# Kernel tuning notes

Hardware: AMD Instinct MI355X
Metric: run time of the kernel (lower is better)

Reference implementation:

```python
import jax, jax.numpy as jnp
import numpy as np

# Config (matches init_kwargs): num_ori=0 -> plain ConvNext path, single scale, knn-16 graph.
N, B, G, K = 16384, 8, 2048, 16   # N nodes = B graphs x G nodes, k-NN with self loops
C, BD, WF, L = 128, 128, 4, 4     # hidden, basis_dim, widening_factor, num layers
POLY_IN = 3                        # PolynomialFeatures(degree=2) on [E,1] dist -> [d, d^2, d^3]


def knn_edges(pos):
    # Graphs are contiguous blocks of G nodes (batch = node // G).
    pg = pos.reshape(B, G, 3)
    d2 = jnp.sum((pg[:, :, None, :] - pg[:, None, :, :]) ** 2, axis=-1)  # [B,G,G]
    _, idx = jax.lax.top_k(-d2, K)                                       # [B,G,K] incl. self (loop=True)
    offset = (jnp.arange(B) * G)[:, None, None]
    src = (idx + offset).reshape(-1)            # neighbor (source) node per edge, [E]
    dst = jnp.repeat(jnp.arange(B * G), K)      # center (target) node per edge, [E]
    return src, dst


def layer_norm(h, g, b):
    mu = jnp.mean(h, axis=-1, keepdims=True)
    var = jnp.var(h, axis=-1, keepdims=True)
    return (h - mu) / jnp.sqrt(var + 1e-5) * g + b


def setup_inputs() -> dict:
    key = jax.random.key(0)
    ks = jax.random.split(key, 20)
    s = 0.05
    inp = {
        'x': jax.random.normal(ks[0], (N, 65), jnp.float32),
        'pos': jax.random.normal(ks[1], (N, 3), jnp.float32),
        'batch': jnp.repeat(jnp.arange(B, dtype=jnp.int32), G),
        # x_embedder (no bias)
        'W_embed': jax.random.normal(ks[2], (65, C), jnp.float32) * s,
        # spatial basis MLP: poly(3) -> Linear -> GELU -> Linear -> GELU
        'Wb1': jax.random.normal(ks[3], (POLY_IN, BD), jnp.float32) * s,
        'bb1': jnp.zeros((BD,), jnp.float32),
        'Wb2': jax.random.normal(ks[4], (BD, BD), jnp.float32) * s,
        'bb2': jnp.zeros((BD,), jnp.float32),
        # per-layer ConvNext params (stacked over L layers)
        'Wk': jax.random.normal(ks[5], (L, BD, C), jnp.float32) * s,  # depthwise conv kernel gen
        'ln_g': jnp.ones((L, C), jnp.float32),
        'ln_b': jnp.zeros((L, C), jnp.float32),
        'W1': jax.random.normal(ks[6], (L, C, WF * C), jnp.float32) * s,
        'b1': jnp.zeros((L, WF * C), jnp.float32),
        'W2': jax.random.normal(ks[7], (L, WF * C, C), jnp.float32) * s,
        'b2': jnp.zeros((L, C), jnp.float32),
        # readout
        'Wr': jax.random.normal(ks[8], (C, 1), jnp.float32) * s,
        'br': jnp.zeros((1,), jnp.float32),
    }
    return inp


def reference(x, pos, batch, W_embed, Wb1, bb1, Wb2, bb2, Wk, ln_g, ln_b, W1, b1, W2, b2, Wr, br):
    src, dst = knn_edges(pos)
    # SEn invariant with num_ori=0: pairwise distance (eps for self-loop grad safety)
    diff = pos[src] - pos[dst]                                    # [E,3]
    d = jnp.sqrt(jnp.sum(diff * diff, axis=-1, keepdims=True) + 1e-12)  # [E,1]
    # PolynomialFeatures(degree=2): [d, d^2, d^3]
    poly = jnp.concatenate([d, d * d, d * d * d], axis=-1)        # [E,3]
    kb = jax.nn.gelu(poly @ Wb1 + bb1)
    kernel = jax.nn.gelu(kb @ Wb2 + bb2)                          # [E,BD] spatial kernel basis

    h = x @ W_embed                                               # [N,C]
    for i in range(L):
        # depthwise conv: per-edge kernel from basis, gather-multiply-scatter
        k_i = kernel @ Wk[i]                                      # [E,C]
        msg = h[src] * k_i                                        # [E,C]
        agg = jax.ops.segment_sum(msg, dst, num_segments=N)       # [N,C]
        z = layer_norm(agg, ln_g[i], ln_b[i])
        z = jax.nn.gelu(z @ W1[i] + b1[i]) @ W2[i] + b2[i]        # pointwise inverted-bottleneck
        h = h + z                                                 # residual (in==out channels)
    out = h @ Wr + br                                             # readout, [N,1] scalar output
    return out
```

## Files before the change

### kernel.cpp

```cpp
#include <hip/hip_runtime.h>
#include <hip/hip_bf16.h>

#define NN 16384
#define GG 2048
#define KNN 16
#define EE (NN*KNN)
#define NL 4

typedef _Float16 f16;
typedef _Float16 half8 __attribute__((ext_vector_type(8)));
typedef _Float16 half4 __attribute__((ext_vector_type(4)));
typedef float f32x4 __attribute__((ext_vector_type(4)));
typedef unsigned long long u64;

__device__ __forceinline__ float gelu_tanh(float x) {
  float s = x*x;
  float u = __fmaf_rn(-0.0713548194f, s, -1.5957691216f);
  float p = __expf(x*u);
  return x * __builtin_amdgcn_rcpf(1.0f + p);
}

__device__ __forceinline__ int mbcnt64(u64 m) {
  return __builtin_amdgcn_mbcnt_hi((unsigned)(m >> 32),
         __builtin_amdgcn_mbcnt_lo((unsigned)m, 0));
}

__global__ __launch_bounds__(256) void possoa_kernel(const float* __restrict__ pos,
    float* __restrict__ posx, float* __restrict__ posy, float* __restrict__ posz) {
  int n = blockIdx.x*256 + threadIdx.x;
  posx[n] = pos[(size_t)n*3+0];
  posy[n] = pos[(size_t)n*3+1];
  posz[n] = pos[(size_t)n*3+2];
}

__global__ __launch_bounds__(256) void knn_kernel(const float* __restrict__ posx,
    const float* __restrict__ posy, const float* __restrict__ posz,
    int* __restrict__ srci, float* __restrict__ dedge) {
  __shared__ u64 sel[4][16];
  int tid = threadIdx.x;
  int wv = tid >> 6;
  int node = blockIdx.x*4 + wv;
  int lane = tid & 63;
  int base = node & ~(GG-1);
  float qx = posx[node], qy = posy[node], qz = posz[node];

  float d2s[32];
  float c0 = 3.4e38f, c1 = 3.4e38f, c2 = 3.4e38f, c3 = 3.4e38f;
  #pragma unroll
  for (int it = 0; it < 32; ++it) {
    int j = base + it*64 + lane;
    float dx = __fsub_rn(qx, posx[j]);
    float dy = __fsub_rn(qy, posy[j]);
    float dz = __fsub_rn(qz, posz[j]);
    float d2 = __fadd_rn(__fadd_rn(__fmul_rn(dx,dx), __fmul_rn(dy,dy)), __fmul_rn(dz,dz));
    d2s[it] = d2;
    float x = d2;
    float t0 = fminf(c0, x); x = fmaxf(c0, x); c0 = t0;
    float t1 = fminf(c1, x); x = fmaxf(c1, x); c1 = t1;
    float t2 = fminf(c2, x); x = fmaxf(c2, x); c2 = t2;
    c3 = fminf(c3, x);
  }
  unsigned T = 0;
  for (int b = 30; b >= 0; --b) {
    unsigned tb = T | (1u << b);
    float tf = __uint_as_float(tb);
    int cnt = __popcll(__ballot(c0 < tf)) + __popcll(__ballot(c1 < tf))
            + __popcll(__ballot(c2 < tf)) + __popcll(__ballot(c3 < tf));
    if (cnt < 16) T = tb;
  }
  float Tf = __uint_as_float(T);
  int cless;
  if (!__any(c3 <= Tf)) {
    cless = __popcll(__ballot(c0 < Tf)) + __popcll(__ballot(c1 < Tf))
          + __popcll(__ballot(c2 < Tf)) + __popcll(__ballot(c3 < Tf));
  } else {
    T = 0;
    for (int b = 30; b >= 0; --b) {
      unsigned tb = T | (1u << b);
      float tf = __uint_as_float(tb);
      int cnt = 0;
      #pragma unroll
      for (int q = 0; q < 32; ++q) cnt += __popcll(__ballot(d2s[q] < tf));
      if (cnt < 16) T = tb;
    }
    Tf = __uint_as_float(T);
    cless = 0;
    #pragma unroll
    for (int q = 0; q < 32; ++q) cless += __popcll(__ballot(d2s[q] < Tf));
  }
  int offb = 0;
  int tieq = 16 - cless;
  #pragma unroll
  for (int it = 0; it < 32; ++it) {
    u64 mless = __ballot(d2s[it] < Tf);
    u64 mtie  = __ballot(d2s[it] == Tf);
    bool store = (d2s[it] < Tf);
    int slot = offb + mbcnt64(mless);
    offb += (int)__popcll(mless);
    if (mtie != 0 && tieq > 0) {
      int tr = mbcnt64(mtie);
      if (d2s[it] == Tf && tr < tieq) { store = true; slot = offb + tr; }
      int take = (int)__popcll(mtie); take = take < tieq ? take : tieq;
      offb += take; tieq -= take;
    }
    if (store)
      sel[wv][slot] = ((u64)__float_as_uint(d2s[it]) << 32) | (unsigned)(it*64 + lane);
  }
  if (lane < KNN) {
    u64 e = sel[wv][lane];
    int rank = 0;
    #pragma unroll
    for (int k2 = 0; k2 < 16; ++k2) rank += (sel[wv][k2] < e) ? 1 : 0;
    int j = (int)(e & 0xffffffffu);
    float d2v = __uint_as_float((unsigned)(e >> 32));
    srci[node*KNN + rank] = base + j;
    dedge[node*KNN + rank] = sqrtf(__fadd_rn(d2v, 1e-12f));
  }
}

__global__ __launch_bounds__(256) void prep_kernel(
    const float* __restrict__ Wb2, const float* __restrict__ Wk,
    const float* __restrict__ W1, const float* __restrict__ W2,
    f16* __restrict__ Wb2t, f16* __restrict__ Wkt,
    f16* __restrict__ W1t, f16* __restrict__ W2t) {
  int i = blockIdx.x*256 + threadIdx.x;
  if (i < 16384) {
    int c = i >> 7, k = i & 127;
    Wb2t[i] = (f16)Wb2[k*128 + c];
    return;
  }
  i -= 16384;
  if (i < 65536) {
    int l = i >> 14, r = i & 16383; int c = r >> 7, k = r & 127;
    Wkt[i] = (f16)Wk[l*16384 + k*128 + c];
    return;
  }
  i -= 65536;
  if (i < 262144) {
    int l = i >> 16, r = i & 65535; int c = r >> 7, k = r & 127;
    W1t[i] = (f16)W1[l*65536 + k*512 + c];
    return;
  }
  i -= 262144;
  if (i < 262144) {
    int l = i >> 16, r = i & 65535; int c = r >> 9, k = r & 511;
    W2t[i] = (f16)W2[l*65536 + k*128 + c];
  }
}

__global__ __launch_bounds__(256) void embed_kernel(const float* __restrict__ x,
    const float* __restrict__ We, float* __restrict__ h) {
  int t = threadIdx.x;
  int n = blockIdx.x*8 + (t >> 5);
  int q = (t & 31) * 4;
  f32x4 acc = {0.f,0.f,0.f,0.f};
  const float* xr = x + n*65;
  for (int k = 0; k < 65; ++k) {
    float xv = xr[k];
    f32x4 wv = *(const f32x4*)(We + k*128 + q);
    acc += xv * wv;
  }
  *(f32x4*)(h + (size_t)n*128 + q) = acc;
}

__global__ __launch_bounds__(256) void basis_kernel(const float* __restrict__ dedge,
    const float* __restrict__ Wb1, const float* __restrict__ bb1,
    const f16* __restrict__ Wb2t, const float* __restrict__ bb2,
    f16* __restrict__ kernA) {
  __shared__ f16 Wb2s[128][136];
  __shared__ f16 kb[64][136];
  int t = threadIdx.x;
  #pragma unroll
  for (int it = 0; it < 8; ++it) {
    int idx = it*256 + t;
    int row = idx >> 4, k8 = (idx & 15) * 8;
    *(half8*)&Wb2s[row][k8] = *(const half8*)&Wb2t[row*128 + k8];
  }
  __syncthreads();
  int w = t >> 6, l = t & 63;
  int row4 = l >> 4, rlo = l & 15;
  #pragma unroll
  for (int tt = 0; tt < 2; ++tt) {
    size_t Tg = (size_t)blockIdx.x*8 + (size_t)w*2 + tt;
    float d = dedge[Tg*16 + rlo];
    float d2 = d*d, d3 = d2*d;
    half8 a[4];
    #pragma unroll
    for (int kc = 0; kc < 4; ++kc) {
      int k0 = kc*32 + row4*8;
      f32x4 w1a = *(const f32x4*)&Wb1[k0],     w1b = *(const f32x4*)&Wb1[k0+4];
      f32x4 w2a = *(const f32x4*)&Wb1[128+k0], w2b = *(const f32x4*)&Wb1[128+k0+4];
      f32x4 w3a = *(const f32x4*)&Wb1[256+k0], w3b = *(const f32x4*)&Wb1[256+k0+4];
      f32x4 bba = *(const f32x4*)&bb1[k0],     bbb = *(const f32x4*)&bb1[k0+4];
      #pragma unroll
      for (int j = 0; j < 4; ++j) {
        a[kc][j]   = (f16)gelu_tanh(d*w1a[j] + d2*w2a[j] + d3*w3a[j] + bba[j]);
        a[kc][4+j] = (f16)gelu_tanh(d*w1b[j] + d2*w2b[j] + d3*w3b[j] + bbb[j]);
      }
    }
    f32x4 acc[8];
    #pragma unroll
    for (int nt = 0; nt < 8; ++nt) {
      acc[nt] = (f32x4){0.f,0.f,0.f,0.f};
      #pragma unroll
      for (int kc = 0; kc < 4; ++kc) {
        half8 b = *(const half8*)&Wb2s[nt*16 + rlo][kc*32 + row4*8];
        acc[nt] = __builtin_amdgcn_mfma_f32_16x16x32_f16(a[kc], b, acc[nt], 0, 0, 0);
      }
    }
    #pragma unroll
    for (int nt = 0; nt < 8; ++nt) {
      float bias = bb2[nt*16 + rlo];
      #pragma unroll
      for (int j = 0; j < 4; ++j)
        kb[w*16 + row4*4 + j][nt*16 + rlo] = (f16)gelu_tanh(acc[nt][j] + bias);
    }
    #pragma unroll
    for (int kc = 0; kc < 4; ++kc) {
      half8 v = *(const half8*)&kb[w*16 + rlo][kc*32 + row4*8];
      *(half8*)&kernA[((Tg*4 + kc)*64 + l)*8] = v;
    }
  }
}

__global__ __launch_bounds__(512) void layer_kernel(const f16* __restrict__ kernA,
    const f16* __restrict__ Wkt_l, const int* __restrict__ srci,
    const float* __restrict__ hin,
    const float* __restrict__ lng, const float* __restrict__ lnb,
    const f16* __restrict__ W1t_l, const float* __restrict__ b1_l,
    const f16* __restrict__ W2t_l, const float* __restrict__ b2_l,
    float* __restrict__ hout) {
  __shared__ __align__(16) char smem_u[34816];
  f16 (*Wkts)[136] = (f16(*)[136])smem_u;
  f16 (*y1)[520]   = (f16(*)[520])smem_u;
  __shared__ float aggl[32][132];
  __shared__ f16 zl[32][136];
  int t = threadIdx.x;
  int w = t >> 6, l = t & 63;
  int row4 = l >> 4, rlo = l & 15;
  int n0 = blockIdx.x * 32;

  #pragma unroll
  for (int it = 0; it < 4; ++it) {
    int idx = it*512 + t;
    int row = idx >> 4, k8 = (idx & 15) * 8;
    *(half8*)&Wkts[row][k8] = *(const half8*)&Wkt_l[row*128 + k8];
  }

  int sidxA[4][4];
  #pragma unroll
  for (int m = 0; m < 4; ++m)
    #pragma unroll
    for (int j = 0; j < 4; ++j)
      sidxA[m][j] = srci[(n0 + w*4 + m)*16 + row4*4 + j];
  __syncthreads();

  #pragma unroll
  for (int m = 0; m < 4; ++m) {
    int node = n0 + w*4 + m;
    half8 a[4];
    #pragma unroll
    for (int kc = 0; kc < 4; ++kc)
      a[kc] = *(const half8*)&kernA[(((size_t)node*4 + kc)*64 + l)*8];
    float hv[8][4];
    #pragma unroll
    for (int nt = 0; nt < 8; ++nt)
      #pragma unroll
      for (int j = 0; j < 4; ++j)
        hv[nt][j] = hin[(size_t)sidxA[m][j]*128 + nt*16 + rlo];
    #pragma unroll
    for (int nt = 0; nt < 8; ++nt) {
      half8 bf4[4];
      #pragma unroll
      for (int kc = 0; kc < 4; ++kc)
        bf4[kc] = *(const half8*)&Wkts[nt*16 + rlo][kc*32 + row4*8];
      f32x4 acc = {0.f,0.f,0.f,0.f};
      #pragma unroll
      for (int kc = 0; kc < 4; ++kc)
        acc = __builtin_amdgcn_mfma_f32_16x16x32_f16(a[kc], bf4[kc], acc, 0, 0, 0);
      float p = 0.f;
      #pragma unroll
      for (int j = 0; j < 4; ++j) p += acc[j] * hv[nt][j];
      p += __shfl_xor(p, 16, 64);
      p += __shfl_xor(p, 32, 64);
      if (l < 16) aggl[w*4 + m][nt*16 + l] = p;
    }
  }
  {
    int row = w*4 + row4;
    int cb = rlo*8;
    f32x4 va = *(const f32x4*)&aggl[row][cb];
    f32x4 vb = *(const f32x4*)&aggl[row][cb+4];
    float s = va[0]+va[1]+va[2]+va[3] + vb[0]+vb[1]+vb[2]+vb[3];
    #pragma unroll
    for (int st = 1; st < 16; st <<= 1) s += __shfl_xor(s, st, 64);
    float mu = s * (1.f/128.f);
    f32x4 da = va - mu, db = vb - mu;
    float s2 = da[0]*da[0]+da[1]*da[1]+da[2]*da[2]+da[3]*da[3]
             + db[0]*db[0]+db[1]*db[1]+db[2]*db[2]+db[3]*db[3];
    #pragma unroll
    for (int st = 1; st < 16; st <<= 1) s2 += __shfl_xor(s2, st, 64);
    float inv = rsqrtf(s2*(1.f/128.f) + 1e-5f);
    f32x4 ga = *(const f32x4*)&lng[cb], gb = *(const f32x4*)&lng[cb+4];
    f32x4 ba = *(const f32x4*)&lnb[cb], bb = *(const f32x4*)&lnb[cb+4];
    f32x4 za = da*inv*ga + ba, zb = db*inv*gb + bb;
    half8 hz = { (f16)za[0],(f16)za[1],(f16)za[2],(f16)za[3],
                 (f16)zb[0],(f16)zb[1],(f16)zb[2],(f16)zb[3] };
    *(half8*)&zl[row][cb] = hz;
  }
  __syncthreads();
  half8 aza[4], azb[4];
  #pragma unroll
  for (int kc = 0; kc < 4; ++kc) {
    aza[kc] = *(const half8*)&zl[rlo][kc*32 + row4*8];
    azb[kc] = *(const half8*)&zl[16 + rlo][kc*32 + row4*8];
  }
  #pragma unroll
  for (int ntl = 0; ntl < 4; ++ntl) {
    int col = (w*4 + ntl)*16 + rlo;
    f32x4 accA = {0.f,0.f,0.f,0.f}, accB = {0.f,0.f,0.f,0.f};
    #pragma unroll
    for (int kc = 0; kc < 4; ++kc) {
      half8 b = *(const half8*)&W1t_l[(size_t)col*128 + kc*32 + row4*8];
      accA = __builtin_amdgcn_mfma_f32_16x16x32_f16(aza[kc], b, accA, 0, 0, 0);
      accB = __builtin_amdgcn_mfma_f32_16x16x32_f16(azb[kc], b, accB, 0, 0, 0);
    }
    float bias = b1_l[col];
    #pragma unroll
    for (int j = 0; j < 4; ++j) {
      y1[row4*4 + j][col]      = (f16)gelu_tanh(accA[j] + bias);
      y1[16 + row4*4 + j][col] = (f16)gelu_tanh(accB[j] + bias);
    }
  }
  __syncthreads();
  {
    int col = w*16 + rlo;
    f32x4 accA = {0.f,0.f,0.f,0.f}, accB = {0.f,0.f,0.f,0.f};
    #pragma unroll
    for (int kc2 = 0; kc2 < 16; ++kc2) {
      half8 b   = *(const half8*)&W2t_l[(size_t)col*512 + kc2*32 + row4*8];
      half8 a2a = *(const half8*)&y1[rlo][kc2*32 + row4*8];
      half8 a2b = *(const half8*)&y1[16 + rlo][kc2*32 + row4*8];
      accA = __builtin_amdgcn_mfma_f32_16x16x32_f16(a2a, b, accA, 0, 0, 0);
      accB = __builtin_amdgcn_mfma_f32_16x16x32_f16(a2b, b, accB, 0, 0, 0);
    }
    float bias = b2_l[col];
    #pragma unroll
    for (int j = 0; j < 4; ++j) {
      size_t na = (size_t)(n0 + row4*4 + j);
      size_t nb = (size_t)(n0 + 16 + row4*4 + j);
      hout[na*128 + col] = accA[j] + bias + hin[na*128 + col];
      hout[nb*128 + col] = accB[j] + bias + hin[nb*128 + col];
    }
  }
}

__global__ __launch_bounds__(256) void readout_kernel(const float* __restrict__ h,
    const float* __restrict__ Wr, const float* __restrict__ br, float* __restrict__ out) {
  int n = blockIdx.x*256 + threadIdx.x;
  f32x4 acc = {0.f,0.f,0.f,0.f};
  #pragma unroll
  for (int cb = 0; cb < 32; ++cb) {
    f32x4 hv = *(const f32x4*)(h + (size_t)n*128 + cb*4);
    f32x4 wv = *(const f32x4*)(Wr + cb*4);
    acc += hv*wv;
  }
  out[n] = acc[0]+acc[1]+acc[2]+acc[3] + br[0];
}

extern "C" void kernel_launch(void* const* d_in, const int* in_sizes, int n_in,
                              void* d_out, int out_size, void* d_ws, size_t ws_size,
                              hipStream_t stream) {
  const float* x   = (const float*)d_in[0];
  const float* pos = (const float*)d_in[1];
  const float* We  = (const float*)d_in[3];
  const float* Wb1 = (const float*)d_in[4];
  const float* bb1 = (const float*)d_in[5];
  const float* Wb2 = (const float*)d_in[6];
  const float* bb2 = (const float*)d_in[7];
  const float* Wk  = (const float*)d_in[8];
  const float* lng = (const float*)d_in[9];
  const float* lnb = (const float*)d_in[10];
  const float* W1  = (const float*)d_in[11];
  const float* b1  = (const float*)d_in[12];
  const float* W2  = (const float*)d_in[13];
  const float* b2  = (const float*)d_in[14];
  const float* Wr  = (const float*)d_in[15];
  const float* br  = (const float*)d_in[16];
  float* out = (float*)d_out;

  char* p = (char*)d_ws;
  int*   srci  = (int*)p;     p += (size_t)EE*4;
  float* dedge = (float*)p;   p += (size_t)EE*4;
  f16*   kernA = (f16*)p;     p += (size_t)EE*128*2;
  float* hA    = (float*)p;   p += (size_t)NN*128*4;
  float* hB    = (float*)p;   p += (size_t)NN*128*4;
  f16* Wb2t    = (f16*)p;     p += (size_t)16384*2;
  f16* Wkt     = (f16*)p;     p += (size_t)65536*2;
  f16* W1t     = (f16*)p;     p += (size_t)262144*2;
  f16* W2t     = (f16*)p;     p += (size_t)262144*2;
  float* posx  = (float*)p;   p += (size_t)NN*4;
  float* posy  = (float*)p;   p += (size_t)NN*4;
  float* posz  = (float*)p;   p += (size_t)NN*4;

  possoa_kernel<<<NN/256, 256, 0, stream>>>(pos, posx, posy, posz);
  prep_kernel<<<2368, 256, 0, stream>>>(Wb2, Wk, W1, W2, Wb2t, Wkt, W1t, W2t);
  knn_kernel<<<NN/4, 256, 0, stream>>>(posx, posy, posz, srci, dedge);
  basis_kernel<<<2048, 256, 0, stream>>>(dedge, Wb1, bb1, Wb2t, bb2, kernA);
  embed_kernel<<<NN/8, 256, 0, stream>>>(x, We, hA);
  float* hin = hA;
  for (int lyr = 0; lyr < NL; ++lyr) {
    float* hout = (hin == hA) ? hB : hA;
    layer_kernel<<<NN/32, 512, 0, stream>>>(kernA, Wkt + lyr*16384, srci, hin,
        lng + lyr*128, lnb + lyr*128,
        W1t + (size_t)lyr*65536, b1 + lyr*512, W2t + (size_t)lyr*65536, b2 + lyr*128, hout);
    hin = hout;
  }
  readout_kernel<<<NN/256, 256, 0, stream>>>(hin, Wr, br, out);
}
```

Before: 284.2 us.

## Compute layer norm in registers and cut register pressure in layer kernel

Drops the shared-memory aggregation buffer. Layer-norm statistics are now computed directly from the per-lane partial sums in registers. Neighbor indices are loaded per node instead of all up front, and the h gathers are split into two halves to shrink live registers. A launch_bounds minimum-blocks hint of 6 is added to push occupancy higher. This trades more redundant shuffle reductions and narrower scalar LDS stores for lower LDS and VGPR use, at the risk of spilling if the occupancy hint is too aggressive.

```diff
diff --git a/kernel.cpp b/kernel.cpp
--- a/kernel.cpp
+++ b/kernel.cpp
@@ -223,7 +223,7 @@
   }
 }
 
-__global__ __launch_bounds__(512) void layer_kernel(const f16* __restrict__ kernA,
+__global__ __launch_bounds__(512, 6) void layer_kernel(const f16* __restrict__ kernA,
     const f16* __restrict__ Wkt_l, const int* __restrict__ srci,
     const float* __restrict__ hin,
     const float* __restrict__ lng, const float* __restrict__ lnb,
@@ -233,7 +233,6 @@
   __shared__ __align__(16) char smem_u[34816];
   f16 (*Wkts)[136] = (f16(*)[136])smem_u;
   f16 (*y1)[520]   = (f16(*)[520])smem_u;
-  __shared__ float aggl[32][132];
   __shared__ f16 zl[32][136];
   int t = threadIdx.x;
   int w = t >> 6, l = t & 63;
@@ -246,67 +245,65 @@
     int row = idx >> 4, k8 = (idx & 15) * 8;
     *(half8*)&Wkts[row][k8] = *(const half8*)&Wkt_l[row*128 + k8];
   }
-
-  int sidxA[4][4];
-  #pragma unroll
-  for (int m = 0; m < 4; ++m)
-    #pragma unroll
-    for (int j = 0; j < 4; ++j)
-      sidxA[m][j] = srci[(n0 + w*4 + m)*16 + row4*4 + j];
   __syncthreads();
 
   #pragma unroll
   for (int m = 0; m < 4; ++m) {
     int node = n0 + w*4 + m;
+    int sidx[4];
+    #pragma unroll
+    for (int j = 0; j < 4; ++j)
+      sidx[j] = srci[node*16 + row4*4 + j];
     half8 a[4];
     #pragma unroll
     for (int kc = 0; kc < 4; ++kc)
       a[kc] = *(const half8*)&kernA[(((size_t)node*4 + kc)*64 + l)*8];
-    float hv[8][4];
-    #pragma unroll
-    for (int nt = 0; nt < 8; ++nt)
-      #pragma unroll
-      for (int j = 0; j < 4; ++j)
-        hv[nt][j] = hin[(size_t)sidxA[m][j]*128 + nt*16 + rlo];
-    #pragma unroll
-    for (int nt = 0; nt < 8; ++nt) {
-      half8 bf4[4];
-      #pragma unroll
-      for (int kc = 0; kc < 4; ++kc)
-        bf4[kc] = *(const half8*)&Wkts[nt*16 + rlo][kc*32 + row4*8];
-      f32x4 acc = {0.f,0.f,0.f,0.f};
-      #pragma unroll
-      for (int kc = 0; kc < 4; ++kc)
-        acc = __builtin_amdgcn_mfma_f32_16x16x32_f16(a[kc], bf4[kc], acc, 0, 0, 0);
-      float p = 0.f;
-      #pragma unroll
-      for (int j = 0; j < 4; ++j) p += acc[j] * hv[nt][j];
-      p += __shfl_xor(p, 16, 64);
-      p += __shfl_xor(p, 32, 64);
-      if (l < 16) aggl[w*4 + m][nt*16 + l] = p;
-    }
-  }
-  {
-    int row = w*4 + row4;
-    int cb = rlo*8;
-    f32x4 va = *(const f32x4*)&aggl[row][cb];
-    f32x4 vb = *(const f32x4*)&aggl[row][cb+4];
-    float s = va[0]+va[1]+va[2]+va[3] + vb[0]+vb[1]+vb[2]+vb[3];
+    float ph[8];
+    #pragma unroll
+    for (int hh = 0; hh < 2; ++hh) {
+      float hv[4][4];
+      #pragma unroll
+      for (int nt4 = 0; nt4 < 4; ++nt4)
+        #pragma unroll
+        for (int j = 0; j < 4; ++j)
+          hv[nt4][j] = hin[(size_t)sidx[j]*128 + (hh*4 + nt4)*16 + rlo];
+      #pragma unroll
+      for (int nt4 = 0; nt4 < 4; ++nt4) {
+        half8 bf4[4];
+        #pragma unroll
+        for (int kc = 0; kc < 4; ++kc)
+          bf4[kc] = *(const half8*)&Wkts[(hh*4 + nt4)*16 + rlo][kc*32 + row4*8];
+        f32x4 acc = {0.f,0.f,0.f,0.f};
+        #pragma unroll
+        for (int kc = 0; kc < 4; ++kc)
+          acc = __builtin_amdgcn_mfma_f32_16x16x32_f16(a[kc], bf4[kc], acc, 0, 0, 0);
+        float p = 0.f;
+        #pragma unroll
+        for (int j = 0; j < 4; ++j) p += acc[j] * hv[nt4][j];
+        p += __shfl_xor(p, 16, 64);
+        p += __shfl_xor(p, 32, 64);
+        ph[hh*4 + nt4] = p;
+      }
+    }
+    float s = 0.f;
+    #pragma unroll
+    for (int nt = 0; nt < 8; ++nt) s += ph[nt];
     #pragma unroll
     for (int st = 1; st < 16; st <<= 1) s += __shfl_xor(s, st, 64);
     float mu = s * (1.f/128.f);
-    f32x4 da = va - mu, db = vb - mu;
-    float s2 = da[0]*da[0]+da[1]*da[1]+da[2]*da[2]+da[3]*da[3]
-             + db[0]*db[0]+db[1]*db[1]+db[2]*db[2]+db[3]*db[3];
+    float s2 = 0.f;
+    #pragma unroll
+    for (int nt = 0; nt < 8; ++nt) { float dd = ph[nt] - mu; s2 += dd*dd; }
     #pragma unroll
     for (int st = 1; st < 16; st <<= 1) s2 += __shfl_xor(s2, st, 64);
     float inv = rsqrtf(s2*(1.f/128.f) + 1e-5f);
-    f32x4 ga = *(const f32x4*)&lng[cb], gb = *(const f32x4*)&lng[cb+4];
-    f32x4 ba = *(const f32x4*)&lnb[cb], bb = *(const f32x4*)&lnb[cb+4];
-    f32x4 za = da*inv*ga + ba, zb = db*inv*gb + bb;
-    half8 hz = { (f16)za[0],(f16)za[1],(f16)za[2],(f16)za[3],
-                 (f16)zb[0],(f16)zb[1],(f16)zb[2],(f16)zb[3] };
-    *(half8*)&zl[row][cb] = hz;
+    int row = w*4 + m;
+    #pragma unroll
+    for (int nt = 0; nt < 8; ++nt) {
+      int col = nt*16 + rlo;
+      float z = (ph[nt] - mu)*inv*lng[col] + lnb[col];
+      if (l < 16) zl[row][col] = (f16)z;
+    }
   }
   __syncthreads();
   half8 aza[4], azb[4];
```

Measured after the change: 291.6 us. 2.6% more time.

## Split fused layer kernel into separate conv+layernorm and MLP kernels

Applied to the files above, without the earlier changes.

Splits the per-layer fused kernel into two: one does the depthwise conv gather, aggregation and layer norm, then writes normalized features in f16 MFMA-fragment order to a global buffer. A second kernel reads that buffer and runs the two-matmul MLP with residual. The aim is lower per-kernel register and LDS pressure so more blocks fit per CU. The cost is an extra launch per layer and a global round trip of the normalized activations.

```diff
diff --git a/kernel.cpp b/kernel.cpp
--- a/kernel.cpp
+++ b/kernel.cpp
@@ -223,16 +223,12 @@
   }
 }
 
-__global__ __launch_bounds__(512) void layer_kernel(const f16* __restrict__ kernA,
+__global__ __launch_bounds__(512) void convln_kernel(const f16* __restrict__ kernA,
     const f16* __restrict__ Wkt_l, const int* __restrict__ srci,
     const float* __restrict__ hin,
     const float* __restrict__ lng, const float* __restrict__ lnb,
-    const f16* __restrict__ W1t_l, const float* __restrict__ b1_l,
-    const f16* __restrict__ W2t_l, const float* __restrict__ b2_l,
-    float* __restrict__ hout) {
-  __shared__ __align__(16) char smem_u[34816];
-  f16 (*Wkts)[136] = (f16(*)[136])smem_u;
-  f16 (*y1)[520]   = (f16(*)[520])smem_u;
+    f16* __restrict__ zlg) {
+  __shared__ f16 Wkts[128][136];
   __shared__ float aggl[32][132];
   __shared__ f16 zl[32][136];
   int t = threadIdx.x;
@@ -246,7 +242,6 @@
     int row = idx >> 4, k8 = (idx & 15) * 8;
     *(half8*)&Wkts[row][k8] = *(const half8*)&Wkt_l[row*128 + k8];
   }
-
   int sidxA[4][4];
   #pragma unroll
   for (int m = 0; m < 4; ++m)
@@ -309,11 +304,34 @@
     *(half8*)&zl[row][cb] = hz;
   }
   __syncthreads();
+  {
+    int tile = t >> 8;
+    int kc = (t >> 6) & 3;
+    int ll = t & 63;
+    int r4 = ll >> 4, rl = ll & 15;
+    half8 v = *(const half8*)&zl[tile*16 + rl][kc*32 + r4*8];
+    size_t Tg = (size_t)blockIdx.x*2 + tile;
+    *(half8*)&zlg[((Tg*4 + kc)*64 + ll)*8] = v;
+  }
+}
+
+__global__ __launch_bounds__(512) void mlp_kernel(const f16* __restrict__ zlg,
+    const float* __restrict__ hin,
+    const f16* __restrict__ W1t_l, const float* __restrict__ b1_l,
+    const f16* __restrict__ W2t_l, const float* __restrict__ b2_l,
+    float* __restrict__ hout) {
+  __shared__ f16 y1[32][520];
+  int t = threadIdx.x;
+  int w = t >> 6, l = t & 63;
+  int row4 = l >> 4, rlo = l & 15;
+  int n0 = blockIdx.x * 32;
+  size_t Tg0 = (size_t)blockIdx.x * 2;
+
   half8 aza[4], azb[4];
   #pragma unroll
   for (int kc = 0; kc < 4; ++kc) {
-    aza[kc] = *(const half8*)&zl[rlo][kc*32 + row4*8];
-    azb[kc] = *(const half8*)&zl[16 + rlo][kc*32 + row4*8];
+    aza[kc] = *(const half8*)&zlg[((Tg0*4 + kc)*64 + l)*8];
+    azb[kc] = *(const half8*)&zlg[(((Tg0+1)*4 + kc)*64 + l)*8];
   }
   #pragma unroll
   for (int ntl = 0; ntl < 4; ++ntl) {
@@ -402,6 +420,7 @@
   float* posx  = (float*)p;   p += (size_t)NN*4;
   float* posy  = (float*)p;   p += (size_t)NN*4;
   float* posz  = (float*)p;   p += (size_t)NN*4;
+  f16* zlg     = (f16*)p;     p += (size_t)NN*128*2;
 
   possoa_kernel<<<NN/256, 256, 0, stream>>>(pos, posx, posy, posz);
   prep_kernel<<<2368, 256, 0, stream>>>(Wb2, Wk, W1, W2, Wb2t, Wkt, W1t, W2t);
@@ -411,8 +430,9 @@
   float* hin = hA;
   for (int lyr = 0; lyr < NL; ++lyr) {
     float* hout = (hin == hA) ? hB : hA;
-    layer_kernel<<<NN/32, 512, 0, stream>>>(kernA, Wkt + lyr*16384, srci, hin,
-        lng + lyr*128, lnb + lyr*128,
+    convln_kernel<<<NN/32, 512, 0, stream>>>(kernA, Wkt + lyr*16384, srci, hin,
+        lng + lyr*128, lnb + lyr*128, zlg);
+    mlp_kernel<<<NN/32, 512, 0, stream>>>(zlg, hin,
         W1t + (size_t)lyr*65536, b1 + lyr*512, W2t + (size_t)lyr*65536, b2 + lyr*128, hout);
     hin = hout;
   }
```

New measurement: 309.1 us. 1.09x slower.
